# Optimization experiments

Measured on AMD Instinct MI355X. Metric: run time of the kernel, lower is better.

Reference implementation:

```python
import jax, jax.numpy as jnp
import numpy as np

# --- gate primitives on {0,1}-valued float tensors (same math as the SNN gates) ---
def _AND(a, b):
    return a * b

def _OR(a, b):
    return a + b - a * b

def _NOT(a):
    return 1.0 - a

def _XOR(a, b):
    return a + b - 2.0 * a * b

def _MUX(sel, a, b):
    # sel==1 -> a, sel==0 -> b
    return sel * a + (1.0 - sel) * b


def _ripple_add8(a_lsb, b_lsb):
    """8-bit ripple-carry adder; inputs/outputs LSB-first along last axis."""
    carry = jnp.zeros_like(a_lsb[..., 0:1])
    bits = []
    for i in range(8):  # fixed 8-bit loop, structural not data-dim
        ai = a_lsb[..., i:i + 1]
        bi = b_lsb[..., i:i + 1]
        p = _XOR(ai, bi)
        bits.append(_XOR(p, carry))
        carry = _OR(_AND(ai, bi), _AND(p, carry))
    return jnp.concatenate(bits, axis=-1), carry


def setup_inputs() -> dict:
    key = jax.random.key(0)
    # random 0/1 bit pulses: [N, 8] = [S, E3, E2, E1, E0, M2, M1, M0]
    fp8_pulse = jax.random.randint(key, (4194304, 8), 0, 2).astype(jnp.float32)
    return {"fp8_pulse": fp8_pulse}


def reference(fp8_pulse):
    zeros = jnp.zeros_like(fp8_pulse[..., 0:1])
    ones = jnp.ones_like(zeros)

    s = fp8_pulse[..., 0:1]
    e3 = fp8_pulse[..., 1:2]; e2 = fp8_pulse[..., 2:3]
    e1 = fp8_pulse[..., 3:4]; e0 = fp8_pulse[..., 4:5]
    m2 = fp8_pulse[..., 5:6]; m1 = fp8_pulse[..., 6:7]; m0 = fp8_pulse[..., 7:8]

    # exponent / mantissa zero detection
    e_nonzero = _OR(_OR(e0, e1), _OR(e2, e3))
    e_is_zero = _NOT(e_nonzero)
    m_nonzero = _OR(_OR(m0, m1), m2)
    is_subnormal = _AND(e_is_zero, m_nonzero)

    # normal path: fp32_exp = fp8_exp + 120 (8-bit adder, LSB-first)
    fp8_exp_lsb = jnp.concatenate([e0, e1, e2, e3, zeros, zeros, zeros, zeros], axis=-1)
    const_120_lsb = jnp.concatenate([zeros, zeros, zeros, ones, ones, ones, ones, zeros], axis=-1)
    fp32_exp_raw_lsb, _ = _ripple_add8(fp8_exp_lsb, const_120_lsb)
    fp32_exp_raw = jnp.flip(fp32_exp_raw_lsb, axis=-1)  # MSB-first

    # subnormal mantissa leading-one position
    not_m2 = _NOT(m2)
    not_m1 = _NOT(m1)
    m_is_1xx = m2
    m_is_01x = _AND(not_m2, m1)

    sub_exp_120 = jnp.concatenate([zeros, ones, ones, ones, ones, zeros, zeros, zeros], axis=-1)
    sub_exp_119 = jnp.concatenate([zeros, ones, ones, ones, zeros, ones, ones, ones], axis=-1)
    sub_exp_118 = jnp.concatenate([zeros, ones, ones, ones, zeros, ones, ones, zeros], axis=-1)

    m_is_01x_e = jnp.broadcast_to(m_is_01x, m_is_01x.shape[:-1] + (8,))
    m_is_1xx_e = jnp.broadcast_to(m_is_1xx, m_is_1xx.shape[:-1] + (8,))
    sel_01x_or_001 = _MUX(m_is_01x_e, sub_exp_119, sub_exp_118)
    sub_exp = _MUX(m_is_1xx_e, sub_exp_120, sel_01x_or_001)

    sub_m22 = _OR(_AND(m_is_01x, m0), _AND(m_is_1xx, m1))
    sub_m21 = _AND(m_is_1xx, m0)
    sub_mant = jnp.concatenate([sub_m22, sub_m21] + [zeros] * 21, axis=-1)

    zero_exp = jnp.concatenate([zeros] * 8, axis=-1)
    zero_mant = jnp.concatenate([zeros] * 23, axis=-1)

    is_true_zero = _AND(e_is_zero, _NOT(m_nonzero))

    is_sub_e = jnp.broadcast_to(is_subnormal, is_subnormal.shape[:-1] + (8,))
    is_tz_e = jnp.broadcast_to(is_true_zero, is_true_zero.shape[:-1] + (8,))
    e_normal_or_sub = _MUX(is_sub_e, sub_exp, fp32_exp_raw)
    fp32_exp = _MUX(is_tz_e, zero_exp, e_normal_or_sub)

    normal_mant = jnp.concatenate([m2, m1, m0] + [zeros] * 20, axis=-1)
    is_sub_m = jnp.broadcast_to(is_subnormal, is_subnormal.shape[:-1] + (23,))
    is_tz_m = jnp.broadcast_to(is_true_zero, is_true_zero.shape[:-1] + (23,))
    m_normal_or_sub = _MUX(is_sub_m, sub_mant, normal_mant)
    fp32_mant = _MUX(is_tz_m, zero_mant, m_normal_or_sub)

    return jnp.concatenate([s, fp32_exp, fp32_mant], axis=-1)  # [..., 32]
```

## Files before the change

### kernel.cpp

```cpp
#include <hip/hip_runtime.h>


typedef unsigned int u32x4 __attribute__((ext_vector_type(4)));

__global__ __launch_bounds__(256) void fp8_bits_to_fp32_bits(
    const u32x4* __restrict__ in,
    u32x4* __restrict__ out,
    int n4)
{
    const unsigned ONE = 0x3F800000u;
    const int stride = gridDim.x * blockDim.x;
    const int gid0 = blockIdx.x * blockDim.x + threadIdx.x;

    for (int base = gid0; base < n4; base += stride * 4) {
        u32x4 lo[4], hi[4];
        bool valid[4];

#pragma unroll
        for (int k = 0; k < 4; ++k) {
            int gid = base + k * stride;
            valid[k] = gid < n4;
            if (valid[k]) {
                int row = gid >> 3;
                lo[k] = in[row * 2 + 0];
                hi[k] = in[row * 2 + 1];
            }
        }

#pragma unroll
        for (int k = 0; k < 4; ++k) {
            if (!valid[k]) continue;
            int gid = base + k * stride;
            int sub = gid & 7;

            unsigned s31 = (lo[k].x << 8) & 0x80000000u;
            unsigned e = ((lo[k].y >> 20) & 8u) | ((lo[k].z >> 21) & 4u) |
                         ((lo[k].w >> 22) & 2u) | ((hi[k].x >> 23) & 1u);
            unsigned m = ((hi[k].y >> 21) & 4u) | ((hi[k].z >> 22) & 2u) |
                         ((hi[k].w >> 23) & 1u);

            unsigned u;
            if (e != 0u)        u = ((e + 120u) << 23) | (m << 20);
            else if (m & 4u)    u = (120u << 23) | ((m & 3u) << 21);
            else if (m & 2u)    u = (119u << 23) | ((m & 1u) << 22);
            else if (m & 1u)    u = (118u << 23);
            else                u = 0u;
            u |= s31;

            int i0 = sub << 2;
            u32x4 o;
            o.x = ((u >> (31 - (i0 + 0))) & 1u) ? ONE : 0u;
            o.y = ((u >> (31 - (i0 + 1))) & 1u) ? ONE : 0u;
            o.z = ((u >> (31 - (i0 + 2))) & 1u) ? ONE : 0u;
            o.w = ((u >> (31 - (i0 + 3))) & 1u) ? ONE : 0u;

            __builtin_nontemporal_store(o, &out[gid]);
        }
    }
}

extern "C" void kernel_launch(void* const* d_in, const int* in_sizes, int n_in,
                              void* d_out, int out_size, void* d_ws, size_t ws_size,
                              hipStream_t stream) {
    const u32x4* in = (const u32x4*)d_in[0];
    u32x4* out = (u32x4*)d_out;
    int n4 = out_size / 4;
    int block = 256;
    int grid = 2048;
    fp8_bits_to_fp32_bits<<<grid, block, 0, stream>>>(in, out, n4);
}
```

Before: 129.9 us.

## Gather fp8 row bits via wave ballot instead of redundant per-thread row loads

Each thread now loads only the single input float that matches its output index. The 8 bits of a row are then assembled across lanes with __ballot, bit-reversal and a shift, rather than every thread loading the whole 32-byte row. This removes the eight-fold redundant vector loads per row and shrinks per-thread register use. It relies on rows being aligned to 8-lane groups within a wavefront. The per-thread unroll also drops from 4 to 2 items, which lowers the number of memory requests in flight in a kernel that is mostly bandwidth-bound.

```diff
diff --git a/kernel.cpp b/kernel.cpp
--- a/kernel.cpp
+++ b/kernel.cpp
@@ -3,58 +3,58 @@
 
 typedef unsigned int u32x4 __attribute__((ext_vector_type(4)));
 
+__device__ __forceinline__ unsigned decode_u(unsigned packed) {
+    unsigned e = (packed >> 3) & 15u;
+    unsigned m = packed & 7u;
+    unsigned u;
+    if (e != 0u)        u = ((e + 120u) << 23) | (m << 20);
+    else if (m & 4u)    u = (120u << 23) | ((m & 3u) << 21);
+    else if (m & 2u)    u = (119u << 23) | ((m & 1u) << 22);
+    else if (m & 1u)    u = (118u << 23);
+    else                u = 0u;
+    return u | ((packed & 0x80u) << 24);
+}
+
 __global__ __launch_bounds__(256) void fp8_bits_to_fp32_bits(
-    const u32x4* __restrict__ in,
+    const unsigned* __restrict__ in,
     u32x4* __restrict__ out,
     int n4)
 {
     const unsigned ONE = 0x3F800000u;
     const int stride = gridDim.x * blockDim.x;
-    const int gid0 = blockIdx.x * blockDim.x + threadIdx.x;
+    const unsigned lane = threadIdx.x & 63u;
+    const unsigned shamt = lane & 56u;
+    const int i0 = (int)((lane & 7u) << 2);
 
-    for (int base = gid0; base < n4; base += stride * 4) {
-        u32x4 lo[4], hi[4];
-        bool valid[4];
+    for (int gid = blockIdx.x * blockDim.x + threadIdx.x; gid < n4;
+         gid += 2 * stride) {
+        int gidB = gid + stride;
+        unsigned wA = in[gid];
+        unsigned wB = (gidB < n4) ? in[gidB] : 0u;
 
-#pragma unroll
-        for (int k = 0; k < 4; ++k) {
-            int gid = base + k * stride;
-            valid[k] = gid < n4;
-            if (valid[k]) {
-                int row = gid >> 3;
-                lo[k] = in[row * 2 + 0];
-                hi[k] = in[row * 2 + 1];
-            }
-        }
+        unsigned long long mA = __ballot(wA != 0u);
+        unsigned long long mB = __ballot(wB != 0u);
 
-#pragma unroll
-        for (int k = 0; k < 4; ++k) {
-            if (!valid[k]) continue;
-            int gid = base + k * stride;
-            int sub = gid & 7;
+        unsigned pA = __brev((unsigned)(mA >> shamt) & 0xFFu) >> 24;
+        unsigned pB = __brev((unsigned)(mB >> shamt) & 0xFFu) >> 24;
 
-            unsigned s31 = (lo[k].x << 8) & 0x80000000u;
-            unsigned e = ((lo[k].y >> 20) & 8u) | ((lo[k].z >> 21) & 4u) |
-                         ((lo[k].w >> 22) & 2u) | ((hi[k].x >> 23) & 1u);
-            unsigned m = ((hi[k].y >> 21) & 4u) | ((hi[k].z >> 22) & 2u) |
-                         ((hi[k].w >> 23) & 1u);
+        unsigned uA = decode_u(pA);
+        unsigned uB = decode_u(pB);
 
-            unsigned u;
-            if (e != 0u)        u = ((e + 120u) << 23) | (m << 20);
-            else if (m & 4u)    u = (120u << 23) | ((m & 3u) << 21);
-            else if (m & 2u)    u = (119u << 23) | ((m & 1u) << 22);
-            else if (m & 1u)    u = (118u << 23);
-            else                u = 0u;
-            u |= s31;
+        u32x4 oA;
+        oA.x = ((uA >> (31 - (i0 + 0))) & 1u) ? ONE : 0u;
+        oA.y = ((uA >> (31 - (i0 + 1))) & 1u) ? ONE : 0u;
+        oA.z = ((uA >> (31 - (i0 + 2))) & 1u) ? ONE : 0u;
+        oA.w = ((uA >> (31 - (i0 + 3))) & 1u) ? ONE : 0u;
+        __builtin_nontemporal_store(oA, &out[gid]);
 
-            int i0 = sub << 2;
-            u32x4 o;
-            o.x = ((u >> (31 - (i0 + 0))) & 1u) ? ONE : 0u;
-            o.y = ((u >> (31 - (i0 + 1))) & 1u) ? ONE : 0u;
-            o.z = ((u >> (31 - (i0 + 2))) & 1u) ? ONE : 0u;
-            o.w = ((u >> (31 - (i0 + 3))) & 1u) ? ONE : 0u;
-
-            __builtin_nontemporal_store(o, &out[gid]);
+        if (gidB < n4) {
+            u32x4 oB;
+            oB.x = ((uB >> (31 - (i0 + 0))) & 1u) ? ONE : 0u;
+            oB.y = ((uB >> (31 - (i0 + 1))) & 1u) ? ONE : 0u;
+            oB.z = ((uB >> (31 - (i0 + 2))) & 1u) ? ONE : 0u;
+            oB.w = ((uB >> (31 - (i0 + 3))) & 1u) ? ONE : 0u;
+            __builtin_nontemporal_store(oB, &out[gidB]);
         }
     }
 }
@@ -62,7 +62,7 @@
 extern "C" void kernel_launch(void* const* d_in, const int* in_sizes, int n_in,
                               void* d_out, int out_size, void* d_ws, size_t ws_size,
                               hipStream_t stream) {
-    const u32x4* in = (const u32x4*)d_in[0];
+    const unsigned* in = (const unsigned*)d_in[0];
     u32x4* out = (u32x4*)d_out;
     int n4 = out_size / 4;
     int block = 256;
```

After: 105.8 us. -18.6%, faster.
